# Kernel optimization log

Measured on AMD Instinct MI355X. Metric: run time of the kernel, lower is better.

## Reference

```python
import jax, jax.numpy as jnp
import numpy as np

N = 50000
E = 625000
D_IN = 128
D_OUT = 128


def setup_inputs() -> dict:
    key = jax.random.key(0)
    k1, k2, k3, k4 = jax.random.split(key, 4)
    x = jax.random.normal(k1, (N, D_IN), dtype=jnp.float32)
    edge_index = jax.random.randint(k2, (2, E), 0, N, dtype=jnp.int64)
    edge_weight = jax.random.uniform(k3, (E,), dtype=jnp.float32)
    # xavier_uniform with gain=0.05: limit = gain * sqrt(6/(fan_in+fan_out))
    limit = 0.05 * np.sqrt(6.0 / (D_IN + D_OUT))
    weight = jax.random.uniform(k4, (D_OUT, D_IN), dtype=jnp.float32,
                                minval=-limit, maxval=limit)
    bias = jnp.zeros((D_OUT,), dtype=jnp.float32)
    return {"x": x, "edge_index": edge_index, "edge_weight": edge_weight,
            "weight": weight, "bias": bias}


def reference(x, edge_index, edge_weight, weight, bias):
    src = edge_index[0]
    dst = edge_index[1]
    # gather source features and weight per edge: [E, D_IN]
    msg = x[src] * edge_weight[:, None]
    # scatter-add into destination nodes: [N, D_IN]
    agg = jax.ops.segment_sum(msg, dst, num_segments=x.shape[0])
    # linear + bias + relu
    h = agg @ weight.T + bias
    return jax.nn.relu(h)
```

## Files before the change

kernel.cpp:

```cpp
#include <hip/hip_runtime.h>
#include <hip/hip_fp16.h>

#define NN 50000
#define NE 625000
#define D  128
#define CAP 64
#define NBIN 196
#define BCAP 4096
#define BIN_BLOCKS 200
#define BIN_CHUNK 3125
#define GBM 128
#define PREP_BLKS 3125
#define MEGA_X  BIN_BLOCKS
#define MEGA_W  (BIN_BLOCKS + PREP_BLKS)
#define MEGA_GRID (MEGA_W + 8)

typedef __attribute__((ext_vector_type(8))) short bf16x8;
typedef __attribute__((ext_vector_type(4))) float f32x4;

__device__ inline unsigned f2bf_rne(float f) {
    unsigned u = __float_as_uint(f);
    u += 0x7FFFu + ((u >> 16) & 1u);
    return u >> 16;
}

__device__ inline unsigned pack_hi(float a, float b, float& ra, float& rb) {
    unsigned ba = __float_as_uint(a) & 0xffff0000u;
    unsigned bb = __float_as_uint(b) & 0xffff0000u;
    ra = a - __uint_as_float(ba);
    rb = b - __uint_as_float(bb);
    return (ba >> 16) | bb;
}
__device__ inline unsigned pack_lo(float ra, float rb) {
    return (__float_as_uint(ra) >> 16) | (__float_as_uint(rb) & 0xffff0000u);
}

__global__ __launch_bounds__(256) void mega1(const float* __restrict__ x,
                                             const float* __restrict__ W,
                                             const int* __restrict__ src,
                                             const int* __restrict__ dst,
                                             const float* __restrict__ ew,
                                             unsigned* __restrict__ xb,
                                             ushort* __restrict__ wsp,
                                             int* __restrict__ binc,
                                             uint2* __restrict__ binbuf,
                                             int* __restrict__ ovf_cnt,
                                             uint2* __restrict__ ovf) {
    const int tid = threadIdx.x;
    if (blockIdx.x < MEGA_X) {
        __shared__ int hcnt[4][NBIN];
        __shared__ int hbase[NBIN];
        __shared__ int hcur[NBIN];
        const int wv = tid >> 6;
        const int e0 = blockIdx.x * BIN_CHUNK;
        const int e1 = min(e0 + BIN_CHUNK, NE);
        for (int i = tid; i < NBIN; i += 256) {
            hcnt[0][i] = 0; hcnt[1][i] = 0; hcnt[2][i] = 0; hcnt[3][i] = 0;
        }
        __syncthreads();
        for (int e = e0 + tid; e < e1; e += 256)
            atomicAdd(&hcnt[wv][dst[e] >> 8], 1);
        __syncthreads();
        for (int i = tid; i < NBIN; i += 256) {
            int c = hcnt[0][i] + hcnt[1][i] + hcnt[2][i] + hcnt[3][i];
            hbase[i] = c ? atomicAdd(&binc[i], c) : 0;
            hcur[i] = 0;
        }
        __syncthreads();
        for (int e = e0 + tid; e < e1; e += 256) {
            int d = dst[e];
            int bin = d >> 8;
            unsigned entry = ((unsigned)src[e] << 16) |
                             (unsigned)__half_as_ushort(__float2half(ew[e]));
            int slot = hbase[bin] + atomicAdd(&hcur[bin], 1);
            if (slot < BCAP) {
                binbuf[(size_t)bin * BCAP + slot] = make_uint2((unsigned)d, entry);
            } else {
                int o = atomicAdd(ovf_cnt, 1);
                ovf[o] = make_uint2((unsigned)d, entry);
            }
        }
        return;
    }
    if (blockIdx.x < MEGA_W) {
        int g = (blockIdx.x - MEGA_X) * 256 + tid;
        const float4* xp = (const float4*)(x + (size_t)g * 8);
        float4 a = xp[0], b = xp[1];
        uint4 o;
        o.x = f2bf_rne(a.x) | (f2bf_rne(a.y) << 16);
        o.y = f2bf_rne(a.z) | (f2bf_rne(a.w) << 16);
        o.z = f2bf_rne(b.x) | (f2bf_rne(b.y) << 16);
        o.w = f2bf_rne(b.z) | (f2bf_rne(b.w) << 16);
        ((uint4*)xb)[g] = o;
        return;
    }
    int g = (blockIdx.x - MEGA_W) * 256 + tid;
    if (g >= 128 * 16) return;
    int col = g >> 4;
    int c16 = g & 15;
    const float4* wp = (const float4*)(W + (size_t)col * D + c16 * 8);
    float4 v0 = wp[0], v1 = wp[1];
    float r0, r1, r2, r3, r4, r5, r6, r7;
    uint4 hi, lo;
    hi.x = pack_hi(v0.x, v0.y, r0, r1);
    hi.y = pack_hi(v0.z, v0.w, r2, r3);
    hi.z = pack_hi(v1.x, v1.y, r4, r5);
    hi.w = pack_hi(v1.z, v1.w, r6, r7);
    lo.x = pack_lo(r0, r1); lo.y = pack_lo(r2, r3);
    lo.z = pack_lo(r4, r5); lo.w = pack_lo(r6, r7);
    int sidx = col * 16 + (c16 ^ (col & 15));
    ((uint4*)wsp)[sidx] = hi;
    ((uint4*)(wsp + 16384))[sidx] = lo;
}

__global__ __launch_bounds__(256) void bin_fill(const int* __restrict__ binc,
                                                const uint2* __restrict__ binbuf,
                                                int* __restrict__ fillc,
                                                unsigned* __restrict__ buck,
                                                int* __restrict__ ovf_cnt,
                                                uint2* __restrict__ ovf) {
    __shared__ int lcnt[256];
    const int tid = threadIdx.x;
    const int bin = blockIdx.x;
    lcnt[tid] = 0;
    __syncthreads();
    int n = binc[bin];
    if (n > BCAP) n = BCAP;
    const uint2* bp = binbuf + (size_t)bin * BCAP;
    for (int i = tid; i < n; i += 256) {
        uint2 q = bp[i];
        int d = (int)q.x;
        int p = atomicAdd(&lcnt[d & 255], 1);
        if (p < CAP) {
            buck[(size_t)d * CAP + p] = q.y;
        } else {
            int o = atomicAdd(ovf_cnt, 1);
            ovf[o] = q;
        }
    }
    __syncthreads();
    int node = bin * 256 + tid;
    if (node < NN) {
        int c = lcnt[tid];
        if (c > CAP) c = CAP;
        int pc = (c + 3) & ~3;
        for (int p = c; p < pc; ++p)
            buck[(size_t)node * CAP + p] = 0;
        fillc[node] = pc;
    }
}

__global__ __launch_bounds__(256) void aggregate(const unsigned* __restrict__ xb,
                                                 const int* __restrict__ fillc,
                                                 const unsigned* __restrict__ buck,
                                                 const int* __restrict__ ovf_cnt,
                                                 const uint2* __restrict__ ovf,
                                                 unsigned* __restrict__ aggb) {
    const int node = blockIdx.x * 8 + (threadIdx.x >> 5);
    const int t = threadIdx.x & 31;
    int cnt = fillc[node];
    if (cnt > CAP) cnt = CAP;
    const uint4* bp4 = (const uint4*)(buck + (size_t)node * CAP);
    const uint2* x2 = (const uint2*)xb;
    float4 acc = {0.f, 0.f, 0.f, 0.f};
    int n4 = cnt >> 2;
    for (int i = 0; i < n4; ++i) {
        uint4 q = bp4[i];
        uint2 u0 = x2[(size_t)(q.x >> 16) * 32 + t];
        uint2 u1 = x2[(size_t)(q.y >> 16) * 32 + t];
        uint2 u2 = x2[(size_t)(q.z >> 16) * 32 + t];
        uint2 u3 = x2[(size_t)(q.w >> 16) * 32 + t];
        float w0 = __half2float(__ushort_as_half((ushort)(q.x & 0xffffu)));
        float w1 = __half2float(__ushort_as_half((ushort)(q.y & 0xffffu)));
        float w2 = __half2float(__ushort_as_half((ushort)(q.z & 0xffffu)));
        float w3 = __half2float(__ushort_as_half((ushort)(q.w & 0xffffu)));
        acc.x += __uint_as_float(u0.x << 16) * w0;
        acc.y += __uint_as_float(u0.x & 0xffff0000u) * w0;
        acc.z += __uint_as_float(u0.y << 16) * w0;
        acc.w += __uint_as_float(u0.y & 0xffff0000u) * w0;
        acc.x += __uint_as_float(u1.x << 16) * w1;
        acc.y += __uint_as_float(u1.x & 0xffff0000u) * w1;
        acc.z += __uint_as_float(u1.y << 16) * w1;
        acc.w += __uint_as_float(u1.y & 0xffff0000u) * w1;
        acc.x += __uint_as_float(u2.x << 16) * w2;
        acc.y += __uint_as_float(u2.x & 0xffff0000u) * w2;
        acc.z += __uint_as_float(u2.y << 16) * w2;
        acc.w += __uint_as_float(u2.y & 0xffff0000u) * w2;
        acc.x += __uint_as_float(u3.x << 16) * w3;
        acc.y += __uint_as_float(u3.x & 0xffff0000u) * w3;
        acc.z += __uint_as_float(u3.y << 16) * w3;
        acc.w += __uint_as_float(u3.y & 0xffff0000u) * w3;
    }
    int n = *ovf_cnt;
    for (int o = 0; o < n; ++o) {
        uint2 q = ovf[o];
        if ((int)q.x == node) {
            uint2 u = x2[(size_t)(q.y >> 16) * 32 + t];
            float w = __half2float(__ushort_as_half((ushort)(q.y & 0xffffu)));
            acc.x += __uint_as_float(u.x << 16) * w;
            acc.y += __uint_as_float(u.x & 0xffff0000u) * w;
            acc.z += __uint_as_float(u.y << 16) * w;
            acc.w += __uint_as_float(u.y & 0xffff0000u) * w;
        }
    }
    unsigned o0 = f2bf_rne(acc.x) | (f2bf_rne(acc.y) << 16);
    unsigned o1 = f2bf_rne(acc.z) | (f2bf_rne(acc.w) << 16);
    ((uint2*)aggb)[(size_t)node * 32 + t] = make_uint2(o0, o1);
}

__global__ __launch_bounds__(256) void gemm_mfma(const unsigned* __restrict__ aggb,
                                                 const ushort* __restrict__ wsp,
                                                 const float* __restrict__ bias,
                                                 float* __restrict__ out) {
    __shared__ ushort wl[32768];
    const int tid = threadIdx.x;
    {
        const uint4* s = (const uint4*)wsp;
        uint4* d = (uint4*)wl;
#pragma unroll
        for (int i = 0; i < 16; ++i)
            d[i * 256 + tid] = s[i * 256 + tid];
    }
    __syncthreads();

    const int wid = tid >> 6, lane = tid & 63;
    const int l15 = lane & 15, kg = lane >> 4;
    const int wrbase = blockIdx.x * GBM + wid * 32;

    f32x4 acc[2][8];
    const f32x4 fz = {0.f, 0.f, 0.f, 0.f};
#pragma unroll
    for (int m = 0; m < 2; ++m)
#pragma unroll
        for (int n = 0; n < 8; ++n) acc[m][n] = fz;

    int arow0 = wrbase + l15;
    int arow1 = wrbase + 16 + l15;
    const unsigned* a0p = aggb + (size_t)(arow0 < NN ? arow0 : NN - 1) * 64 + kg * 4;
    const unsigned* a1p = aggb + (size_t)(arow1 < NN ? arow1 : NN - 1) * 64 + kg * 4;

#pragma unroll
    for (int kk = 0; kk < 4; ++kk) {
        uint4 h0 = *(const uint4*)(a0p + kk * 16);
        uint4 h1 = *(const uint4*)(a1p + kk * 16);
        bf16x8 a0 = *(bf16x8*)&h0;
        bf16x8 a1 = *(bf16x8*)&h1;

        int coff = ((kk * 4 + kg) ^ l15) * 8;
#pragma unroll
        for (int nf = 0; nf < 8; ++nf) {
            int bidx = (16 * nf + l15) * 128 + coff;
            bf16x8 bhi = *(const bf16x8*)&wl[bidx];
            bf16x8 blo = *(const bf16x8*)&wl[16384 + bidx];
            acc[0][nf] = __builtin_amdgcn_mfma_f32_16x16x32_bf16(a0, bhi, acc[0][nf], 0, 0, 0);
            acc[1][nf] = __builtin_amdgcn_mfma_f32_16x16x32_bf16(a1, bhi, acc[1][nf], 0, 0, 0);
            acc[0][nf] = __builtin_amdgcn_mfma_f32_16x16x32_bf16(a0, blo, acc[0][nf], 0, 0, 0);
            acc[1][nf] = __builtin_amdgcn_mfma_f32_16x16x32_bf16(a1, blo, acc[1][nf], 0, 0, 0);
        }
    }

    const int rofs = kg * 4;
#pragma unroll
    for (int nf = 0; nf < 8; ++nf) {
        int col = 16 * nf + l15;
        float bv = bias[col];
#pragma unroll
        for (int m = 0; m < 2; ++m) {
#pragma unroll
            for (int r = 0; r < 4; ++r) {
                int row = wrbase + 16 * m + rofs + r;
                if (row < NN) {
                    float h = acc[m][nf][r] + bv;
                    out[(size_t)row * D + col] = h > 0.f ? h : 0.f;
                }
            }
        }
    }
}

extern "C" void kernel_launch(void* const* d_in, const int* in_sizes, int n_in,
                              void* d_out, int out_size, void* d_ws, size_t ws_size,
                              hipStream_t stream) {
    const float* x    = (const float*)d_in[0];
    const int*   eidx = (const int*)d_in[1];
    const float* ew   = (const float*)d_in[2];
    const float* W    = (const float*)d_in[3];
    const float* bias = (const float*)d_in[4];
    float* out = (float*)d_out;

    const int* src = eidx;
    const int* dst = eidx + NE;

    char* base = (char*)d_ws;
    unsigned* aggb   = (unsigned*)base;
    uint2*    binbuf = (uint2*)base;
    unsigned* buck   = (unsigned*)(base + 25600000);
    unsigned* xb     = (unsigned*)(base + 25600000 + 12800000);
    ushort*   wsp    = (ushort*)(base + 51200000);
    int*      fillc   = (int*)(base + 51200000 + 65536);
    int*      binc    = (int*)(base + 51200000 + 65536 + 200000);
    int*      ovf_cnt = (int*)((char*)binc + NBIN * 4);
    uint2*    ovf     = (uint2*)(base + 51200000 + 65536 + 200000 + 1024);

    hipMemsetAsync(binc, 0, NBIN * 4 + 4, stream);
    mega1<<<MEGA_GRID, 256, 0, stream>>>(x, W, src, dst, ew, xb, wsp, binc, binbuf, ovf_cnt, ovf);
    bin_fill<<<NBIN, 256, 0, stream>>>(binc, binbuf, fillc, buck, ovf_cnt, ovf);
    aggregate<<<6250, 256, 0, stream>>>(xb, fillc, buck, ovf_cnt, ovf, aggb);
    gemm_mfma<<<(NN + GBM - 1) / GBM, 256, 0, stream>>>(aggb, wsp, bias, out);
}
```

Baseline: 79.72 us.

## Move x/W conversion into bin-fill kernel and add padded 16-edge fast path

The x and W bf16 conversions move out of the coarse binning kernel and into the fine bucket-fill kernel, so that conversion overlaps with the latency-bound bucket fill instead of the binning pass. Coarse binning now uses per-wave base offsets to cut contention on the shared-memory cursor atomics. Nodes with at most 16 edges are zero-padded to 16, so aggregate can issue all 16 gathers in one unrolled batch for more memory-level parallelism. In exchange, padded zero entries cause extra redundant gathers (of node 0's row) and extra bucket stores.

Measured after the change: 82.33 us. 3.3% more time.

```diff
diff --git a/kernel.cpp b/kernel.cpp
--- a/kernel.cpp
+++ b/kernel.cpp
@@ -10,10 +10,10 @@
 #define BIN_BLOCKS 200
 #define BIN_CHUNK 3125
 #define GBM 128
-#define PREP_BLKS 3125
-#define MEGA_X  BIN_BLOCKS
-#define MEGA_W  (BIN_BLOCKS + PREP_BLKS)
-#define MEGA_GRID (MEGA_W + 8)
+#define XC_BLKS 3125
+#define K2_X  NBIN
+#define K2_W  (NBIN + XC_BLKS)
+#define K2_GRID (K2_W + 8)
 
 typedef __attribute__((ext_vector_type(8))) short bf16x8;
 typedef __attribute__((ext_vector_type(4))) float f32x4;
@@ -35,55 +35,98 @@
     return (__float_as_uint(ra) >> 16) | (__float_as_uint(rb) & 0xffff0000u);
 }
 
-__global__ __launch_bounds__(256) void mega1(const float* __restrict__ x,
-                                             const float* __restrict__ W,
-                                             const int* __restrict__ src,
-                                             const int* __restrict__ dst,
-                                             const float* __restrict__ ew,
-                                             unsigned* __restrict__ xb,
-                                             ushort* __restrict__ wsp,
-                                             int* __restrict__ binc,
-                                             uint2* __restrict__ binbuf,
-                                             int* __restrict__ ovf_cnt,
-                                             uint2* __restrict__ ovf) {
+__global__ __launch_bounds__(256) void bin_coarse(const int* __restrict__ src,
+                                                  const int* __restrict__ dst,
+                                                  const float* __restrict__ ew,
+                                                  int* __restrict__ binc,
+                                                  uint2* __restrict__ binbuf,
+                                                  int* __restrict__ ovf_cnt,
+                                                  uint2* __restrict__ ovf) {
+    __shared__ int hcnt[4][NBIN];
+    __shared__ int hbase4[4][NBIN];
+    __shared__ int hcur4[4][NBIN];
     const int tid = threadIdx.x;
-    if (blockIdx.x < MEGA_X) {
-        __shared__ int hcnt[4][NBIN];
-        __shared__ int hbase[NBIN];
-        __shared__ int hcur[NBIN];
-        const int wv = tid >> 6;
-        const int e0 = blockIdx.x * BIN_CHUNK;
-        const int e1 = min(e0 + BIN_CHUNK, NE);
-        for (int i = tid; i < NBIN; i += 256) {
-            hcnt[0][i] = 0; hcnt[1][i] = 0; hcnt[2][i] = 0; hcnt[3][i] = 0;
-        }
+    const int wv = tid >> 6;
+    const int e0 = blockIdx.x * BIN_CHUNK;
+    const int e1 = min(e0 + BIN_CHUNK, NE);
+
+    for (int i = tid; i < NBIN; i += 256) {
+        hcnt[0][i] = 0; hcnt[1][i] = 0; hcnt[2][i] = 0; hcnt[3][i] = 0;
+    }
+    __syncthreads();
+    for (int e = e0 + tid; e < e1; e += 256)
+        atomicAdd(&hcnt[wv][dst[e] >> 8], 1);
+    __syncthreads();
+    for (int i = tid; i < NBIN; i += 256) {
+        int c0 = hcnt[0][i], c1 = hcnt[1][i], c2 = hcnt[2][i], c3 = hcnt[3][i];
+        int tot = c0 + c1 + c2 + c3;
+        int base = tot ? atomicAdd(&binc[i], tot) : 0;
+        hbase4[0][i] = base;
+        hbase4[1][i] = base + c0;
+        hbase4[2][i] = base + c0 + c1;
+        hbase4[3][i] = base + c0 + c1 + c2;
+        hcur4[0][i] = 0; hcur4[1][i] = 0; hcur4[2][i] = 0; hcur4[3][i] = 0;
+    }
+    __syncthreads();
+    for (int e = e0 + tid; e < e1; e += 256) {
+        int d = dst[e];
+        int bin = d >> 8;
+        unsigned entry = ((unsigned)src[e] << 16) |
+                         (unsigned)__half_as_ushort(__float2half(ew[e]));
+        int slot = hbase4[wv][bin] + atomicAdd(&hcur4[wv][bin], 1);
+        if (slot < BCAP) {
+            binbuf[(size_t)bin * BCAP + slot] = make_uint2((unsigned)d, entry);
+        } else {
+            int o = atomicAdd(ovf_cnt, 1);
+            ovf[o] = make_uint2((unsigned)d, entry);
+        }
+    }
+}
+
+__global__ __launch_bounds__(256) void k2(const float* __restrict__ x,
+                                          const float* __restrict__ W,
+                                          const int* __restrict__ binc,
+                                          const uint2* __restrict__ binbuf,
+                                          int* __restrict__ fillc,
+                                          unsigned* __restrict__ buck,
+                                          unsigned* __restrict__ xb,
+                                          ushort* __restrict__ wsp,
+                                          int* __restrict__ ovf_cnt,
+                                          uint2* __restrict__ ovf) {
+    const int tid = threadIdx.x;
+    if (blockIdx.x < K2_X) {
+        __shared__ int lcnt[256];
+        const int bin = blockIdx.x;
+        lcnt[tid] = 0;
         __syncthreads();
-        for (int e = e0 + tid; e < e1; e += 256)
-            atomicAdd(&hcnt[wv][dst[e] >> 8], 1);
-        __syncthreads();
-        for (int i = tid; i < NBIN; i += 256) {
-            int c = hcnt[0][i] + hcnt[1][i] + hcnt[2][i] + hcnt[3][i];
-            hbase[i] = c ? atomicAdd(&binc[i], c) : 0;
-            hcur[i] = 0;
-        }
-        __syncthreads();
-        for (int e = e0 + tid; e < e1; e += 256) {
-            int d = dst[e];
-            int bin = d >> 8;
-            unsigned entry = ((unsigned)src[e] << 16) |
-                             (unsigned)__half_as_ushort(__float2half(ew[e]));
-            int slot = hbase[bin] + atomicAdd(&hcur[bin], 1);
-            if (slot < BCAP) {
-                binbuf[(size_t)bin * BCAP + slot] = make_uint2((unsigned)d, entry);
+        int n = binc[bin];
+        if (n > BCAP) n = BCAP;
+        const uint2* bp = binbuf + (size_t)bin * BCAP;
+        for (int i = tid; i < n; i += 256) {
+            uint2 q = bp[i];
+            int d = (int)q.x;
+            int p = atomicAdd(&lcnt[d & 255], 1);
+            if (p < CAP) {
+                buck[(size_t)d * CAP + p] = q.y;
             } else {
                 int o = atomicAdd(ovf_cnt, 1);
-                ovf[o] = make_uint2((unsigned)d, entry);
+                ovf[o] = q;
             }
         }
+        __syncthreads();
+        int node = bin * 256 + tid;
+        if (node < NN) {
+            int c = lcnt[tid];
+            if (c > CAP) c = CAP;
+            int pc = (c <= 16) ? 16 : ((c + 3) & ~3);
+            for (int p = c; p < pc; ++p)
+                buck[(size_t)node * CAP + p] = 0;
+            fillc[node] = pc;
+        }
         return;
     }
-    if (blockIdx.x < MEGA_W) {
-        int g = (blockIdx.x - MEGA_X) * 256 + tid;
+    if (blockIdx.x < K2_W) {
+        int g = (blockIdx.x - K2_X) * 256 + tid;
         const float4* xp = (const float4*)(x + (size_t)g * 8);
         float4 a = xp[0], b = xp[1];
         uint4 o;
@@ -94,7 +137,7 @@
         ((uint4*)xb)[g] = o;
         return;
     }
-    int g = (blockIdx.x - MEGA_W) * 256 + tid;
+    int g = (blockIdx.x - K2_W) * 256 + tid;
     if (g >= 128 * 16) return;
     int col = g >> 4;
     int c16 = g & 15;
@@ -113,41 +156,15 @@
     ((uint4*)(wsp + 16384))[sidx] = lo;
 }
 
-__global__ __launch_bounds__(256) void bin_fill(const int* __restrict__ binc,
-                                                const uint2* __restrict__ binbuf,
-                                                int* __restrict__ fillc,
-                                                unsigned* __restrict__ buck,
-                                                int* __restrict__ ovf_cnt,
-                                                uint2* __restrict__ ovf) {
-    __shared__ int lcnt[256];
-    const int tid = threadIdx.x;
-    const int bin = blockIdx.x;
-    lcnt[tid] = 0;
-    __syncthreads();
-    int n = binc[bin];
-    if (n > BCAP) n = BCAP;
-    const uint2* bp = binbuf + (size_t)bin * BCAP;
-    for (int i = tid; i < n; i += 256) {
-        uint2 q = bp[i];
-        int d = (int)q.x;
-        int p = atomicAdd(&lcnt[d & 255], 1);
-        if (p < CAP) {
-            buck[(size_t)d * CAP + p] = q.y;
-        } else {
-            int o = atomicAdd(ovf_cnt, 1);
-            ovf[o] = q;
-        }
-    }
-    __syncthreads();
-    int node = bin * 256 + tid;
-    if (node < NN) {
-        int c = lcnt[tid];
-        if (c > CAP) c = CAP;
-        int pc = (c + 3) & ~3;
-        for (int p = c; p < pc; ++p)
-            buck[(size_t)node * CAP + p] = 0;
-        fillc[node] = pc;
-    }
+__device__ inline float hw(unsigned q) {
+    return __half2float(__ushort_as_half((ushort)(q & 0xffffu)));
+}
+
+__device__ inline void edge_fma(float4& acc, uint2 u, float wt) {
+    acc.x += __uint_as_float(u.x << 16) * wt;
+    acc.y += __uint_as_float(u.x & 0xffff0000u) * wt;
+    acc.z += __uint_as_float(u.y << 16) * wt;
+    acc.w += __uint_as_float(u.y & 0xffff0000u) * wt;
 }
 
 __global__ __launch_bounds__(256) void aggregate(const unsigned* __restrict__ xb,
@@ -159,48 +176,53 @@
     const int node = blockIdx.x * 8 + (threadIdx.x >> 5);
     const int t = threadIdx.x & 31;
     int cnt = fillc[node];
-    if (cnt > CAP) cnt = CAP;
     const uint4* bp4 = (const uint4*)(buck + (size_t)node * CAP);
     const uint2* x2 = (const uint2*)xb;
     float4 acc = {0.f, 0.f, 0.f, 0.f};
-    int n4 = cnt >> 2;
-    for (int i = 0; i < n4; ++i) {
-        uint4 q = bp4[i];
-        uint2 u0 = x2[(size_t)(q.x >> 16) * 32 + t];
-        uint2 u1 = x2[(size_t)(q.y >> 16) * 32 + t];
-        uint2 u2 = x2[(size_t)(q.z >> 16) * 32 + t];
-        uint2 u3 = x2[(size_t)(q.w >> 16) * 32 + t];
-        float w0 = __half2float(__ushort_as_half((ushort)(q.x & 0xffffu)));
-        float w1 = __half2float(__ushort_as_half((ushort)(q.y & 0xffffu)));
-        float w2 = __half2float(__ushort_as_half((ushort)(q.z & 0xffffu)));
-        float w3 = __half2float(__ushort_as_half((ushort)(q.w & 0xffffu)));
-        acc.x += __uint_as_float(u0.x << 16) * w0;
-        acc.y += __uint_as_float(u0.x & 0xffff0000u) * w0;
-        acc.z += __uint_as_float(u0.y << 16) * w0;
-        acc.w += __uint_as_float(u0.y & 0xffff0000u) * w0;
-        acc.x += __uint_as_float(u1.x << 16) * w1;
-        acc.y += __uint_as_float(u1.x & 0xffff0000u) * w1;
-        acc.z += __uint_as_float(u1.y << 16) * w1;
-        acc.w += __uint_as_float(u1.y & 0xffff0000u) * w1;
-        acc.x += __uint_as_float(u2.x << 16) * w2;
-        acc.y += __uint_as_float(u2.x & 0xffff0000u) * w2;
-        acc.z += __uint_as_float(u2.y << 16) * w2;
-        acc.w += __uint_as_float(u2.y & 0xffff0000u) * w2;
-        acc.x += __uint_as_float(u3.x << 16) * w3;
-        acc.y += __uint_as_float(u3.x & 0xffff0000u) * w3;
-        acc.z += __uint_as_float(u3.y << 16) * w3;
-        acc.w += __uint_as_float(u3.y & 0xffff0000u) * w3;
+    if (cnt <= 16) {
+        uint4 q0 = bp4[0], q1 = bp4[1], q2 = bp4[2], q3 = bp4[3];
+        uint2 u00 = x2[(size_t)(q0.x >> 16) * 32 + t];
+        uint2 u01 = x2[(size_t)(q0.y >> 16) * 32 + t];
+        uint2 u02 = x2[(size_t)(q0.z >> 16) * 32 + t];
+        uint2 u03 = x2[(size_t)(q0.w >> 16) * 32 + t];
+        uint2 u10 = x2[(size_t)(q1.x >> 16) * 32 + t];
+        uint2 u11 = x2[(size_t)(q1.y >> 16) * 32 + t];
+        uint2 u12 = x2[(size_t)(q1.z >> 16) * 32 + t];
+        uint2 u13 = x2[(size_t)(q1.w >> 16) * 32 + t];
+        uint2 u20 = x2[(size_t)(q2.x >> 16) * 32 + t];
+        uint2 u21 = x2[(size_t)(q2.y >> 16) * 32 + t];
+        uint2 u22 = x2[(size_t)(q2.z >> 16) * 32 + t];
+        uint2 u23 = x2[(size_t)(q2.w >> 16) * 32 + t];
+        uint2 u30 = x2[(size_t)(q3.x >> 16) * 32 + t];
+        uint2 u31 = x2[(size_t)(q3.y >> 16) * 32 + t];
+        uint2 u32 = x2[(size_t)(q3.z >> 16) * 32 + t];
+        uint2 u33 = x2[(size_t)(q3.w >> 16) * 32 + t];
+        edge_fma(acc, u00, hw(q0.x)); edge_fma(acc, u01, hw(q0.y));
+        edge_fma(acc, u02, hw(q0.z)); edge_fma(acc, u03, hw(q0.w));
+        edge_fma(acc, u10, hw(q1.x)); edge_fma(acc, u11, hw(q1.y));
+        edge_fma(acc, u12, hw(q1.z)); edge_fma(acc, u13, hw(q1.w));
+        edge_fma(acc, u20, hw(q2.x)); edge_fma(acc, u21, hw(q2.y));
+        edge_fma(acc, u22, hw(q2.z)); edge_fma(acc, u23, hw(q2.w));
+        edge_fma(acc, u30, hw(q3.x)); edge_fma(acc, u31, hw(q3.y));
+        edge_fma(acc, u32, hw(q3.z)); edge_fma(acc, u33, hw(q3.w));
+    } else {
+        int n4 = cnt >> 2;
+        for (int i = 0; i < n4; ++i) {
+            uint4 q = bp4[i];
+            uint2 u0 = x2[(size_t)(q.x >> 16) * 32 + t];
+            uint2 u1 = x2[(size_t)(q.y >> 16) * 32 + t];
+            uint2 u2 = x2[(size_t)(q.z >> 16) * 32 + t];
+            uint2 u3 = x2[(size_t)(q.w >> 16) * 32 + t];
+            edge_fma(acc, u0, hw(q.x)); edge_fma(acc, u1, hw(q.y));
+            edge_fma(acc, u2, hw(q.z)); edge_fma(acc, u3, hw(q.w));
+        }
     }
     int n = *ovf_cnt;
     for (int o = 0; o < n; ++o) {
         uint2 q = ovf[o];
         if ((int)q.x == node) {
             uint2 u = x2[(size_t)(q.y >> 16) * 32 + t];
-            float w = __half2float(__ushort_as_half((ushort)(q.y & 0xffffu)));
-            acc.x += __uint_as_float(u.x << 16) * w;
-            acc.y += __uint_as_float(u.x & 0xffff0000u) * w;
-            acc.z += __uint_as_float(u.y << 16) * w;
-            acc.w += __uint_as_float(u.y & 0xffff0000u) * w;
+            edge_fma(acc, u, hw(q.y));
         }
     }
     unsigned o0 = f2bf_rne(acc.x) | (f2bf_rne(acc.y) << 16);
@@ -303,8 +325,8 @@
     uint2*    ovf     = (uint2*)(base + 51200000 + 65536 + 200000 + 1024);
 
     hipMemsetAsync(binc, 0, NBIN * 4 + 4, stream);
-    mega1<<<MEGA_GRID, 256, 0, stream>>>(x, W, src, dst, ew, xb, wsp, binc, binbuf, ovf_cnt, ovf);
-    bin_fill<<<NBIN, 256, 0, stream>>>(binc, binbuf, fillc, buck, ovf_cnt, ovf);
+    bin_coarse<<<BIN_BLOCKS, 256, 0, stream>>>(src, dst, ew, binc, binbuf, ovf_cnt, ovf);
+    k2<<<K2_GRID, 256, 0, stream>>>(x, W, binc, binbuf, fillc, buck, xb, wsp, ovf_cnt, ovf);
     aggregate<<<6250, 256, 0, stream>>>(xb, fillc, buck, ovf_cnt, ovf, aggb);
     gemm_mfma<<<(NN + GBM - 1) / GBM, 256, 0, stream>>>(aggb, wsp, bias, out);
 }
```
